# Kernel optimization log

Hardware: AMD Instinct MI355X
Metric: run time of the kernel (lower is better)

## Reference

```python
import math
import jax, jax.numpy as jnp
import numpy as np

D_MODEL = 1024
N_HEADS = 16
D_K = D_MODEL // N_HEADS


def _alibi_slopes(n_heads):
    # Faithful to the torch _get_slopes: slopes[i] = 2**(-8 + i), subsampled if
    # n_heads is not a power of two.
    power = 2 ** math.ceil(math.log2(n_heads))
    slopes = np.array([2.0 ** (-8 + i) for i in range(power)], dtype=np.float32)
    if n_heads != power:
        ratio = power // n_heads
        slopes = slopes[np.arange(0, power, ratio)][:n_heads]
    return jnp.asarray(slopes)


def setup_inputs() -> dict:
    key = jax.random.key(0)
    ks = jax.random.split(key, 11)
    B, S, D = 2, 2048, D_MODEL
    w = 0.02  # weight init scale
    return {
        "query": jax.random.normal(ks[0], (B, S, D), jnp.float32),
        "key": jax.random.normal(ks[1], (B, S, D), jnp.float32),
        "value": jax.random.normal(ks[2], (B, S, D), jnp.float32),
        "Wq": jax.random.normal(ks[3], (D, D), jnp.float32) * w,
        "bq": jax.random.normal(ks[4], (D,), jnp.float32) * w,
        "Wk": jax.random.normal(ks[5], (D, D), jnp.float32) * w,
        "bk": jax.random.normal(ks[6], (D,), jnp.float32) * w,
        "Wv": jax.random.normal(ks[7], (D, D), jnp.float32) * w,
        "bv": jax.random.normal(ks[8], (D,), jnp.float32) * w,
        "Wo": jax.random.normal(ks[9], (D, D), jnp.float32) * w,
        "bo": jax.random.normal(ks[10], (D,), jnp.float32) * w,
    }


def reference(query, key, value, Wq, bq, Wk, bk, Wv, bv, Wo, bo):
    B, Sq, D = query.shape
    Sk = key.shape[1]
    H, dk = N_HEADS, D_K

    # projections (torch Linear: x @ W.T + b)
    q = (query @ Wq.T + bq).reshape(B, Sq, H, dk).transpose(0, 2, 1, 3)  # [B,H,Sq,dk]
    k = (key @ Wk.T + bk).reshape(B, Sk, H, dk).transpose(0, 2, 1, 3)    # [B,H,Sk,dk]
    v = (value @ Wv.T + bv).reshape(B, Sk, H, dk).transpose(0, 2, 1, 3)  # [B,H,Sk,dk]

    scores = jnp.einsum("bhqd,bhkd->bhqk", q, k) / jnp.sqrt(jnp.float32(dk))

    # ALiBi bias: slopes[h] * (i - j), non-causal path (is_causal=False)
    dist = (jnp.arange(Sq)[:, None] - jnp.arange(Sk)[None, :]).astype(scores.dtype)
    slopes = _alibi_slopes(H)
    scores = scores + slopes[None, :, None, None] * dist[None, None, :, :]

    attn = jax.nn.softmax(scores, axis=-1)
    out = jnp.einsum("bhqk,bhkd->bhqd", attn, v)          # [B,H,Sq,dk]
    out = out.transpose(0, 2, 1, 3).reshape(B, Sq, D)     # [B,Sq,D]
    return out @ Wo.T + bo
```

## Files before the change

kernel.cpp:

```cpp
#include <hip/hip_runtime.h>

typedef __bf16 bf16_t;
typedef bf16_t bf16x8 __attribute__((ext_vector_type(8)));
typedef float f32x4 __attribute__((ext_vector_type(4)));
typedef float f32x16 __attribute__((ext_vector_type(16)));
typedef unsigned short u16x4 __attribute__((ext_vector_type(4)));
typedef unsigned int u32x4v __attribute__((ext_vector_type(4)));
typedef unsigned int u32;

#define DEV static __device__ __forceinline__


DEV unsigned short f2bf(float f) {
  unsigned int u = __builtin_bit_cast(unsigned int, f);
  u = (u + 0x7fffu + ((u >> 16) & 1u)) >> 16;
  return (unsigned short)u;
}

DEV float fexp2(float x) {
  float r;
  asm("v_exp_f32 %0, %1" : "=v"(r) : "v"(x));
  return r;
}

DEV u32 cvtpk(float lo, float hi_) {
  u32 r;
  asm("v_cvt_pk_bf16_f32 %0, %1, %2" : "=v"(r) : "v"(lo), "v"(hi_));
  return r;
}

DEV void plswap(u32& a, u32& b) {
  asm("v_permlane32_swap_b32 %0, %1" : "+v"(a), "+v"(b));
}

DEV void async_ld16(const unsigned short* gsrc, unsigned short* lbase, int lane) {
#if __has_builtin(__builtin_amdgcn_global_load_lds)
  __builtin_amdgcn_global_load_lds(
      (const __attribute__((address_space(1))) unsigned int*)(const void*)gsrc,
      (__attribute__((address_space(3))) unsigned int*)(void*)lbase, 16, 0, 0);
#else
  *reinterpret_cast<u32x4v*>(reinterpret_cast<char*>(lbase) + lane * 16) =
      *reinterpret_cast<const u32x4v*>(gsrc);
#endif
}


DEV void cvt_body(const float* __restrict__ src, unsigned short* __restrict__ dst, int i) {
  const float4* s = reinterpret_cast<const float4*>(src) + (size_t)i * 2;
  float4 a = s[0], c = s[1];
  u16x4 lo = {f2bf(a.x), f2bf(a.y), f2bf(a.z), f2bf(a.w)};
  u16x4 hi = {f2bf(c.x), f2bf(c.y), f2bf(c.z), f2bf(c.w)};
  u16x4* d = reinterpret_cast<u16x4*>(dst) + (size_t)i * 2;
  d[0] = lo;
  d[1] = hi;
}

__global__ __launch_bounds__(256) void cvt_qkv(const float* __restrict__ q,
                                               const float* __restrict__ k,
                                               const float* __restrict__ v,
                                               unsigned short* dq, unsigned short* dk,
                                               unsigned short* dv) {
  const int i = blockIdx.x * 256 + threadIdx.x;
  const float* src = blockIdx.z == 0 ? q : blockIdx.z == 1 ? k : v;
  unsigned short* dst = blockIdx.z == 0 ? dq : blockIdx.z == 1 ? dk : dv;
  cvt_body(src, dst, i);
}

__global__ __launch_bounds__(256) void cvt_w(const float* __restrict__ a,
                                             const float* __restrict__ b,
                                             const float* __restrict__ c,
                                             const float* __restrict__ d, unsigned short* da,
                                             unsigned short* db_, unsigned short* dc,
                                             unsigned short* dd) {
  const int i = blockIdx.x * 256 + threadIdx.x;
  const float* src = blockIdx.z == 0 ? a : blockIdx.z == 1 ? b : blockIdx.z == 2 ? c : d;
  unsigned short* dst = blockIdx.z == 0 ? da : blockIdx.z == 1 ? db_ : blockIdx.z == 2 ? dc : dd;
  cvt_body(src, dst, i);
}


DEV void stage_tile_128x64(const unsigned short* __restrict__ G, int row0, int k0,
                           unsigned short* lbuf, int lane, int wv) {
#pragma unroll
  for (int r = 0; r < 4; ++r) {
    const int rowA = (r * 4 + wv) * 8 + (lane >> 3);
    const int chunk = (lane & 7) ^ (rowA & 7);
    const unsigned short* gsrc = G + (size_t)(row0 + rowA) * 1024 + k0 + chunk * 8;
    unsigned short* lbase = lbuf + (r * 4 + wv) * 512;
    async_ld16(gsrc, lbase, lane);
  }
}

DEV void gemm_core(const unsigned short* __restrict__ X, const unsigned short* __restrict__ W,
                   unsigned short* lA0, unsigned short* lA1, unsigned short* lB0,
                   unsigned short* lB1, int bm0, int bn0, int lane, int wv, int wm, int wn,
                   f32x4 acc[4][4]) {
  stage_tile_128x64(X, bm0, 0, lA0, lane, wv);
  stage_tile_128x64(W, bn0, 0, lB0, lane, wv);
  __syncthreads();
  for (int kt = 0; kt < 16; ++kt) {
    unsigned short* lA = (kt & 1) ? lA1 : lA0;
    unsigned short* lB = (kt & 1) ? lB1 : lB0;
    unsigned short* nA = (kt & 1) ? lA0 : lA1;
    unsigned short* nB = (kt & 1) ? lB0 : lB1;
    if (kt < 15) {
      stage_tile_128x64(X, bm0, (kt + 1) * 64, nA, lane, wv);
      stage_tile_128x64(W, bn0, (kt + 1) * 64, nB, lane, wv);
    }
#pragma unroll
    for (int kk = 0; kk < 2; ++kk) {
      bf16x8 af[4], bfr[4];
#pragma unroll
      for (int f = 0; f < 4; ++f) {
        const int rowA = wm * 64 + f * 16 + (lane & 15);
        const int cA = (kk * 4 + (lane >> 4)) ^ (rowA & 7);
        af[f] = *reinterpret_cast<const bf16x8*>(lA + rowA * 64 + cA * 8);
        const int rowB = wn * 64 + f * 16 + (lane & 15);
        const int cB = (kk * 4 + (lane >> 4)) ^ (rowB & 7);
        bfr[f] = *reinterpret_cast<const bf16x8*>(lB + rowB * 64 + cB * 8);
      }
#pragma unroll
      for (int i = 0; i < 4; ++i)
#pragma unroll
        for (int j = 0; j < 4; ++j)
          acc[i][j] = __builtin_amdgcn_mfma_f32_16x16x32_bf16(af[i], bfr[j], acc[i][j], 0, 0, 0);
    }
    __syncthreads();
  }
}


__global__ __launch_bounds__(256) void gemm_qkv_kernel(
    const unsigned short* __restrict__ Xq, const unsigned short* __restrict__ Xk,
    const unsigned short* __restrict__ Xv, const unsigned short* __restrict__ Wq,
    const unsigned short* __restrict__ Wk, const unsigned short* __restrict__ Wv,
    const float* __restrict__ bq, const float* __restrict__ bk, const float* __restrict__ bv,
    unsigned short* __restrict__ Qp, unsigned short* __restrict__ Kp,
    unsigned short* __restrict__ Vp) {
  __shared__ unsigned short lA[2][128 * 64];
  __shared__ unsigned short lB[2][128 * 64];
  const unsigned short* X;
  const unsigned short* W;
  const float* bias;
  unsigned short* dst;
  if (blockIdx.z == 0) { X = Xq; W = Wq; bias = bq; dst = Qp; }
  else if (blockIdx.z == 1) { X = Xk; W = Wk; bias = bk; dst = Kp; }
  else { X = Xv; W = Wv; bias = bv; dst = Vp; }
  const bool zV = (blockIdx.z == 2);
  const int lane = threadIdx.x & 63, wv = threadIdx.x >> 6;
  const int wm = wv >> 1, wn = wv & 1;
  const int bm0 = blockIdx.x * 128, bn0 = blockIdx.y * 128;
  f32x4 acc[4][4] = {};
  gemm_core(X, W, lA[0], lA[1], lB[0], lB[1], bm0, bn0, lane, wv, wm, wn, acc);
#pragma unroll
  for (int i = 0; i < 4; ++i) {
    const int mbase = bm0 + wm * 64 + i * 16 + ((lane >> 4) << 2);
#pragma unroll
    for (int j = 0; j < 4; ++j) {
      const int n = bn0 + wn * 64 + j * 16 + (lane & 15);
      const float bia = bias[n];
      const int h = n >> 6, d = n & 63;
#pragma unroll
      for (int r = 0; r < 4; ++r) {
        const int m = mbase + r;
        const int b = m >> 11, s = m & 2047;
        const unsigned short val = f2bf(acc[i][j][r] + bia);
        if (zV)
          dst[((size_t)(b * 16 + h) * 64 + d) * 2048 + s] = val;
        else
          dst[((size_t)(b * 16 + h) * 2048 + s) * 64 + d] = val;
      }
    }
  }
}


__global__ __launch_bounds__(256) void gemm_out_kernel(const unsigned short* __restrict__ X,
                                                       const unsigned short* __restrict__ W,
                                                       const float* __restrict__ bias,
                                                       float* __restrict__ out) {
  __shared__ unsigned short lA[2][128 * 64];
  __shared__ unsigned short lB[2][128 * 64];
  const int lane = threadIdx.x & 63, wv = threadIdx.x >> 6;
  const int wm = wv >> 1, wn = wv & 1;
  const int bm0 = blockIdx.x * 128, bn0 = blockIdx.y * 128;
  f32x4 acc[4][4] = {};
  gemm_core(X, W, lA[0], lA[1], lB[0], lB[1], bm0, bn0, lane, wv, wm, wn, acc);
#pragma unroll
  for (int i = 0; i < 4; ++i) {
    const int mbase = bm0 + wm * 64 + i * 16 + ((lane >> 4) << 2);
#pragma unroll
    for (int j = 0; j < 4; ++j) {
      const int n = bn0 + wn * 64 + j * 16 + (lane & 15);
      const float bia = bias[n];
#pragma unroll
      for (int r = 0; r < 4; ++r) out[(size_t)(mbase + r) * 1024 + n] = acc[i][j][r] + bia;
    }
  }
}


__global__ __launch_bounds__(256) void knorm_kernel(const unsigned short* __restrict__ Kp,
                                                    unsigned* __restrict__ nb2) {
  const int bh = blockIdx.y;
  const int s = blockIdx.x * 256 + threadIdx.x;
  const u32x4v* row = reinterpret_cast<const u32x4v*>(Kp + ((size_t)bh * 2048 + s) * 64);
  float ss = 0.0f;
#pragma unroll
  for (int c = 0; c < 8; ++c) {
    u32x4v u = row[c];
#pragma unroll
    for (int e = 0; e < 4; ++e) {
      const float lo = __builtin_bit_cast(float, u[e] << 16);
      const float hi = __builtin_bit_cast(float, u[e] & 0xFFFF0000u);
      ss = __builtin_fmaf(lo, lo, ss);
      ss = __builtin_fmaf(hi, hi, ss);
    }
  }
#pragma unroll
  for (int off = 1; off <= 32; off <<= 1) ss = fmaxf(ss, __shfl_xor(ss, off));
  if ((threadIdx.x & 63) == 0) atomicMax(nb2 + bh, __float_as_uint(ss));
}


__global__ __launch_bounds__(128) void attn_prepass(const unsigned short* __restrict__ Qp,
                                                    const unsigned short* __restrict__ Kp,
                                                    const unsigned* __restrict__ nb2,
                                                    float* __restrict__ mfA,
                                                    float* __restrict__ bltA) {
  __shared__ float sred[4];
  const int lane = threadIdx.x & 63, wv = threadIdx.x >> 6;
  const int lq = lane & 31, hi = lane >> 5;
  const int qt = blockIdx.x, bh = blockIdx.y, h = bh & 15;
  const float L2E = 1.4426950408889634f;
  const float slope2 = ldexpf(L2E, h - 8);
  const float SC2 = 0.125f * L2E;
  const size_t headoff = (size_t)bh * 2048 * 64;
  const unsigned short* Qh = Qp + headoff;
  const unsigned short* Kh = Kp + headoff;
  const int q_glob = qt * 64 + wv * 32 + lq;

  bf16x8 qf[4];
#pragma unroll
  for (int tt = 0; tt < 4; ++tt)
    qf[tt] = *reinterpret_cast<const bf16x8*>(Qh + (size_t)q_glob * 64 + tt * 16 + hi * 8);

  float qq = 0.0f;
#pragma unroll
  for (int tt = 0; tt < 4; ++tt)
#pragma unroll
    for (int e = 0; e < 8; ++e) {
      const float x = (float)qf[tt][e];
      qq = __builtin_fmaf(x, x, qq);
    }
  qq += __shfl_xor(qq, 32);
#pragma unroll
  for (int off = 1; off <= 16; off <<= 1) qq = fmaxf(qq, __shfl_xor(qq, off));

  f32x16 s0 = {}, s1 = {};
#pragma unroll
  for (int tt = 0; tt < 4; ++tt) {
    bf16x8 k0 = *reinterpret_cast<const bf16x8*>(Kh + (size_t)lq * 64 + tt * 16 + hi * 8);
    s0 = __builtin_amdgcn_mfma_f32_32x32x16_bf16(k0, qf[tt], s0, 0, 0, 0);
    bf16x8 k1 = *reinterpret_cast<const bf16x8*>(Kh + (size_t)(32 + lq) * 64 + tt * 16 + hi * 8);
    s1 = __builtin_amdgcn_mfma_f32_32x32x16_bf16(k1, qf[tt], s1, 0, 0, 0);
  }
  float zmax = -3.0e38f;
#pragma unroll
  for (int r = 0; r < 16; ++r) {
    const float cb = -slope2 * (float)(4 * hi + (r & 3) + 8 * (r >> 2));
    const float x0 = __builtin_fmaf(s0[r], SC2, cb);
    const float x1 = __builtin_fmaf(s1[r], SC2, cb - slope2 * 32.0f);
    zmax = fmaxf(zmax, fmaxf(x0, x1));
  }
  zmax = fmaxf(zmax, __shfl_xor(zmax, 32));
  float zmin = zmax;
#pragma unroll
  for (int off = 1; off <= 16; off <<= 1) zmin = fminf(zmin, __shfl_xor(zmin, off));
  if (lane == 0) {
    sred[wv] = zmin;
    sred[2 + wv] = qq;
  }
  __syncthreads();
  if (threadIdx.x == 0) {
    const float mf = fminf(sred[0], sred[1]);
    const float qn = sqrtf(fmaxf(sred[2], sred[3]));
    const float nk = sqrtf(__uint_as_float(nb2[bh]));
    mfA[bh * 32 + qt] = mf;
    bltA[bh * 32 + qt] = qn * nk * SC2;
  }
}


DEV void stage_tile64(const unsigned short* __restrict__ Gbase, size_t stride, int colbase,
                      unsigned short* lbuf, int lane, int wv) {
#pragma unroll
  for (int i = 0; i < 4; ++i) {
    const int r = i * 16 + wv * 8 + (lane >> 3);
    const int chunk = (lane & 7) ^ (r & 7);
    async_ld16(Gbase + (size_t)r * stride + colbase + chunk * 8, lbuf + (i * 16 + wv * 8) * 64,
               lane);
  }
}

__global__ __launch_bounds__(128) void attn_split_kernel(
    const unsigned short* __restrict__ Qp, const unsigned short* __restrict__ Kp,
    const unsigned short* __restrict__ VTp, const float* __restrict__ mfA,
    const float* __restrict__ bltA, float* __restrict__ ML, float* __restrict__ Opart, int Ct,
    int nsplit) {
  __shared__ unsigned short Kb[2][64 * 64];
  __shared__ unsigned short Vb[2][64 * 64];
  const int lane = threadIdx.x & 63, wv = threadIdx.x >> 6;
  const int lq = lane & 31, hi = lane >> 5;
  const int qt = blockIdx.x, sp = blockIdx.y, bh = blockIdx.z;
  const int h = bh & 15;
  const int idx = bh * 32 + qt;
  const float L2E = 1.4426950408889634f;
  const float slope2 = ldexpf(L2E, h - 8);
  const float SC2 = 0.125f * L2E;
  const float m_floor = mfA[idx], blt = bltA[idx];
  const float tf = (blt - m_floor + 34.0f) / (slope2 * 64.0f);
  const int T_act = min(32, (int)tf + 1);
  const int t0 = sp * Ct;
  const int nt = min(Ct, T_act - t0);
  float* mlb = ML + ((size_t)idx * nsplit + sp) * 128;
  if (nt <= 0) {
    mlb[threadIdx.x] = threadIdx.x < 64 ? -3.0e38f : 0.0f;
    return;
  }
  float* ob = Opart + ((size_t)idx * nsplit + sp) * 4096;
  const size_t headoff = (size_t)bh * 2048 * 64;
  const unsigned short* Qh = Qp + headoff;
  const unsigned short* Kh = Kp + headoff;
  const unsigned short* VTh = VTp + headoff;
  const int q_glob = qt * 64 + wv * 32 + lq;

  float cb0[16], cb1[16];
#pragma unroll
  for (int r = 0; r < 16; ++r) {
    cb0[r] = -slope2 * (float)(4 * hi + (r & 3) + 8 * (r >> 2));
    cb1[r] = cb0[r] - slope2 * 32.0f;
  }

  bf16x8 qf[4];
#pragma unroll
  for (int tt = 0; tt < 4; ++tt)
    qf[tt] = *reinterpret_cast<const bf16x8*>(Qh + (size_t)q_glob * 64 + tt * 16 + hi * 8);

  stage_tile64(Kh + (size_t)(t0 * 64) * 64, 64, 0, Kb[0], lane, wv);
  stage_tile64(VTh, 2048, t0 * 64, Vb[0], lane, wv);
  __syncthreads();

  f32x16 acc0 = {}, acc1 = {};
  float m_run = m_floor, l_run = 0.0f;

  for (int ti = 0; ti < nt; ++ti) {
    const int kv0 = (t0 + ti) * 64;
    const float s2k = slope2 * (float)kv0;
    const unsigned short* Kc = Kb[ti & 1];
    const unsigned short* Vc = Vb[ti & 1];
    if (ti + 1 < nt) {
      stage_tile64(Kh + (size_t)(kv0 + 64) * 64, 64, 0, Kb[(ti + 1) & 1], lane, wv);
      stage_tile64(VTh, 2048, kv0 + 64, Vb[(ti + 1) & 1], lane, wv);
    }
    f32x16 s0 = {}, s1 = {};
    __builtin_amdgcn_s_setprio(1);
#pragma unroll
    for (int tt = 0; tt < 4; ++tt) {
      {
        const int row = lq;
        const int ch = (tt * 2 + hi) ^ (row & 7);
        bf16x8 kf = *reinterpret_cast<const bf16x8*>(Kc + row * 64 + ch * 8);
        s0 = __builtin_amdgcn_mfma_f32_32x32x16_bf16(kf, qf[tt], s0, 0, 0, 0);
      }
      {
        const int row = 32 + lq;
        const int ch = (tt * 2 + hi) ^ (row & 7);
        bf16x8 kf = *reinterpret_cast<const bf16x8*>(Kc + row * 64 + ch * 8);
        s1 = __builtin_amdgcn_mfma_f32_32x32x16_bf16(kf, qf[tt], s1, 0, 0, 0);
      }
    }
    __builtin_amdgcn_s_setprio(0);
    float zmax = -3.0e38f;
#pragma unroll
    for (int r = 0; r < 16; ++r) {
      s0[r] = __builtin_fmaf(s0[r], SC2, cb0[r]);
      s1[r] = __builtin_fmaf(s1[r], SC2, cb1[r]);
      zmax = fmaxf(zmax, fmaxf(s0[r], s1[r]));
    }
    zmax = fmaxf(zmax, __shfl_xor(zmax, 32));
    const float tmax_true = zmax - s2k;
    if (__any(tmax_true > m_run + 8.0f)) {
      const float m_new = fmaxf(m_run, tmax_true);
      const float alpha = fexp2(m_run - m_new);
      m_run = m_new;
      l_run *= alpha;
      acc0 *= alpha;
      acc1 *= alpha;
    }
    const float mm = m_run + s2k;
    float ps0 = 0.0f, ps1 = 0.0f;
#pragma unroll
    for (int r = 0; r < 16; ++r) {
      const float p0 = fexp2(s0[r] - mm);
      const float p1 = fexp2(s1[r] - mm);
      s0[r] = p0;
      s1[r] = p1;
      ps0 += p0;
      ps1 += p1;
    }
    float psum = ps0 + ps1;
    psum += __shfl_xor(psum, 32);
    l_run += psum;
    bf16x8 pf[4];
#pragma unroll
    for (int half = 0; half < 2; ++half) {
      u32 w0 = cvtpk(s0[half * 8 + 0], s0[half * 8 + 1]);
      u32 w2 = cvtpk(s0[half * 8 + 4], s0[half * 8 + 5]);
      plswap(w0, w2);
      u32 w1 = cvtpk(s0[half * 8 + 2], s0[half * 8 + 3]);
      u32 w3 = cvtpk(s0[half * 8 + 6], s0[half * 8 + 7]);
      plswap(w1, w3);
      u32x4v ww = {w0, w1, w2, w3};
      pf[half] = __builtin_bit_cast(bf16x8, ww);
    }
#pragma unroll
    for (int half = 0; half < 2; ++half) {
      u32 w0 = cvtpk(s1[half * 8 + 0], s1[half * 8 + 1]);
      u32 w2 = cvtpk(s1[half * 8 + 4], s1[half * 8 + 5]);
      plswap(w0, w2);
      u32 w1 = cvtpk(s1[half * 8 + 2], s1[half * 8 + 3]);
      u32 w3 = cvtpk(s1[half * 8 + 6], s1[half * 8 + 7]);
      plswap(w1, w3);
      u32x4v ww = {w0, w1, w2, w3};
      pf[2 + half] = __builtin_bit_cast(bf16x8, ww);
    }
    __builtin_amdgcn_s_setprio(1);
#pragma unroll
    for (int tt = 0; tt < 4; ++tt) {
      {
        const int row = lq;
        const int ch = (tt * 2 + hi) ^ (row & 7);
        bf16x8 vf = *reinterpret_cast<const bf16x8*>(Vc + row * 64 + ch * 8);
        acc0 = __builtin_amdgcn_mfma_f32_32x32x16_bf16(vf, pf[tt], acc0, 0, 0, 0);
      }
      {
        const int row = 32 + lq;
        const int ch = (tt * 2 + hi) ^ (row & 7);
        bf16x8 vf = *reinterpret_cast<const bf16x8*>(Vc + row * 64 + ch * 8);
        acc1 = __builtin_amdgcn_mfma_f32_32x32x16_bf16(vf, pf[tt], acc1, 0, 0, 0);
      }
    }
    __builtin_amdgcn_s_setprio(0);
    __syncthreads();
  }
  const int qloc = wv * 32 + lq;
  if (hi == 0) {
    mlb[qloc] = m_run;
    mlb[64 + qloc] = l_run;
  }
#pragma unroll
  for (int g = 0; g < 4; ++g) {
    f32x4 w0, w1;
#pragma unroll
    for (int e = 0; e < 4; ++e) {
      w0[e] = acc0[g * 4 + e];
      w1[e] = acc1[g * 4 + e];
    }
    *reinterpret_cast<f32x4*>(ob + qloc * 64 + g * 8 + 4 * hi) = w0;
    *reinterpret_cast<f32x4*>(ob + qloc * 64 + 32 + g * 8 + 4 * hi) = w1;
  }
}


__global__ __launch_bounds__(256) void attn_combine(const float* __restrict__ ML,
                                                    const float* __restrict__ Opart,
                                                    unsigned short* __restrict__ Ob, int nsplit) {
  const int idx = blockIdx.x;
  const int bh = idx >> 5, qt = idx & 31;
  const int h = bh & 15, b = bh >> 4;
  const int q = threadIdx.x >> 2, d0 = (threadIdx.x & 3) * 16;
  const float* mlb = ML + (size_t)idx * nsplit * 128;
  const float* ob = Opart + (size_t)idx * nsplit * 4096;
  float m_g = -3.0e38f;
  for (int s = 0; s < nsplit; ++s) m_g = fmaxf(m_g, mlb[s * 128 + q]);
  float l = 0.0f;
  f32x4 acc[4] = {};
  for (int s = 0; s < nsplit; ++s) {
    const float ms = mlb[s * 128 + q], ls = mlb[s * 128 + 64 + q];
    const float w = fexp2(ms - m_g);
    const float wl = w * ls;
    if (wl > 0.0f) {
      l += wl;
      const f32x4* src = reinterpret_cast<const f32x4*>(ob + (size_t)s * 4096 + q * 64 + d0);
#pragma unroll
      for (int j = 0; j < 4; ++j) {
        f32x4 v = src[j];
#pragma unroll
        for (int e = 0; e < 4; ++e) acc[j][e] = __builtin_fmaf(w, v[e], acc[j][e]);
      }
    }
  }
  const float invl = 1.0f / l;
  unsigned short* orow = Ob + ((size_t)(b * 2048 + qt * 64 + q)) * 1024 + h * 64 + d0;
#pragma unroll
  for (int j = 0; j < 4; ++j) {
    u16x4 pk;
#pragma unroll
    for (int e = 0; e < 4; ++e) pk[e] = f2bf(acc[j][e] * invl);
    *reinterpret_cast<u16x4*>(orow + j * 4) = pk;
  }
}


extern "C" void kernel_launch(void* const* d_in, const int* in_sizes, int n_in, void* d_out,
                              int out_size, void* d_ws, size_t ws_size, hipStream_t stream) {
  const float* q = (const float*)d_in[0];
  const float* k = (const float*)d_in[1];
  const float* v = (const float*)d_in[2];
  const float* Wq = (const float*)d_in[3];
  const float* bq = (const float*)d_in[4];
  const float* Wk = (const float*)d_in[5];
  const float* bk = (const float*)d_in[6];
  const float* Wv = (const float*)d_in[7];
  const float* bv = (const float*)d_in[8];
  const float* Wo = (const float*)d_in[9];
  const float* bo = (const float*)d_in[10];

  char* ws = (char*)d_ws;
  const size_t MB = 1024 * 1024;
  unsigned short* qb = (unsigned short*)(ws + 0 * MB);
  unsigned short* kb = (unsigned short*)(ws + 8 * MB);
  unsigned short* vb = (unsigned short*)(ws + 16 * MB);
  unsigned short* Wqb = (unsigned short*)(ws + 24 * MB);
  unsigned short* Wkb = (unsigned short*)(ws + 26 * MB);
  unsigned short* Wvb = (unsigned short*)(ws + 28 * MB);
  unsigned short* Wob = (unsigned short*)(ws + 30 * MB);
  unsigned short* Qp = (unsigned short*)(ws + 32 * MB);
  unsigned short* Kp = (unsigned short*)(ws + 40 * MB);
  unsigned short* VTp = (unsigned short*)(ws + 48 * MB);
  unsigned short* Obf = (unsigned short*)(ws + 0 * MB);

  int nsplit;
  float *nb2f, *mfA, *bltA, *ML, *Opart;
  if (ws_size >= (size_t)121 * MB) nsplit = 4;
  else if (ws_size >= (size_t)89 * MB) nsplit = 2;
  else nsplit = 1;
  if (ws_size >= (size_t)73 * MB) {
    nb2f = (float*)(ws + 24 * MB);
    mfA = (float*)(ws + 24 * MB + 4096);
    bltA = (float*)(ws + 24 * MB + 8192);
    ML = (float*)(ws + 26 * MB);
    Opart = (float*)(ws + 56 * MB);
  } else {
    nsplit = 1;
    nb2f = (float*)(ws + 26 * MB);
    mfA = (float*)(ws + 26 * MB + 4096);
    bltA = (float*)(ws + 26 * MB + 8192);
    ML = (float*)(ws + 26 * MB + 65536);
    Opart = (float*)(ws + 8 * MB);
  }
  const int Ct = 32 / nsplit;

  cvt_qkv<<<dim3(2048, 1, 3), 256, 0, stream>>>(q, k, v, qb, kb, vb);
  cvt_w<<<dim3(512, 1, 4), 256, 0, stream>>>(Wq, Wk, Wv, Wo, Wqb, Wkb, Wvb, Wob);

  gemm_qkv_kernel<<<dim3(32, 8, 3), 256, 0, stream>>>(qb, kb, vb, Wqb, Wkb, Wvb, bq, bk, bv, Qp,
                                                      Kp, VTp);
  hipMemsetAsync(nb2f, 0, 32 * sizeof(float), stream);
  knorm_kernel<<<dim3(8, 32), 256, 0, stream>>>(Kp, (unsigned*)nb2f);
  attn_prepass<<<dim3(32, 32), 128, 0, stream>>>(Qp, Kp, (const unsigned*)nb2f, mfA, bltA);
  attn_split_kernel<<<dim3(32, nsplit, 32), 128, 0, stream>>>(Qp, Kp, VTp, mfA, bltA, ML, Opart,
                                                              Ct, nsplit);
  attn_combine<<<1024, 256, 0, stream>>>(ML, Opart, Obf, nsplit);
  gemm_out_kernel<<<dim3(32, 8), 256, 0, stream>>>(Obf, Wob, bo, (float*)d_out);
}
```

Before: 131.0 us.

## Merge conversion kernels, shrink GEMM N-tile, swizzle blocks, fold K-norm into QKV GEMM

```diff
diff --git a/kernel.cpp b/kernel.cpp
--- a/kernel.cpp
+++ b/kernel.cpp
@@ -55,48 +55,58 @@
   d[1] = hi;
 }
 
-__global__ __launch_bounds__(256) void cvt_qkv(const float* __restrict__ q,
-                                               const float* __restrict__ k,
-                                               const float* __restrict__ v,
-                                               unsigned short* dq, unsigned short* dk,
-                                               unsigned short* dv) {
-  const int i = blockIdx.x * 256 + threadIdx.x;
-  const float* src = blockIdx.z == 0 ? q : blockIdx.z == 1 ? k : v;
-  unsigned short* dst = blockIdx.z == 0 ? dq : blockIdx.z == 1 ? dk : dv;
+__global__ __launch_bounds__(256) void cvt_all(
+    const float* __restrict__ q, const float* __restrict__ k, const float* __restrict__ v,
+    const float* __restrict__ Wq, const float* __restrict__ Wk, const float* __restrict__ Wv,
+    const float* __restrict__ Wo, unsigned short* dq, unsigned short* dk, unsigned short* dv,
+    unsigned short* dWq, unsigned short* dWk, unsigned short* dWv, unsigned short* dWo) {
+  const int bid = blockIdx.x;
+  const float* src;
+  unsigned short* dst;
+  int i;
+  if (bid < 6144) {
+    const int z = bid >> 11;
+    src = z == 0 ? q : z == 1 ? k : v;
+    dst = z == 0 ? dq : z == 1 ? dk : dv;
+    i = (bid & 2047) * 256 + threadIdx.x;
+  } else {
+    const int z = (bid - 6144) >> 9;
+    src = z == 0 ? Wq : z == 1 ? Wk : z == 2 ? Wv : Wo;
+    dst = z == 0 ? dWq : z == 1 ? dWk : z == 2 ? dWv : dWo;
+    i = ((bid - 6144) & 511) * 256 + threadIdx.x;
+  }
   cvt_body(src, dst, i);
 }
 
-__global__ __launch_bounds__(256) void cvt_w(const float* __restrict__ a,
-                                             const float* __restrict__ b,
-                                             const float* __restrict__ c,
-                                             const float* __restrict__ d, unsigned short* da,
-                                             unsigned short* db_, unsigned short* dc,
-                                             unsigned short* dd) {
-  const int i = blockIdx.x * 256 + threadIdx.x;
-  const float* src = blockIdx.z == 0 ? a : blockIdx.z == 1 ? b : blockIdx.z == 2 ? c : d;
-  unsigned short* dst = blockIdx.z == 0 ? da : blockIdx.z == 1 ? db_ : blockIdx.z == 2 ? dc : dd;
-  cvt_body(src, dst, i);
-}
-
-
-DEV void stage_tile_128x64(const unsigned short* __restrict__ G, int row0, int k0,
-                           unsigned short* lbuf, int lane, int wv) {
+
+DEV void stage_a128(const unsigned short* __restrict__ G, int row0, int k0,
+                    unsigned short* lbuf, int lane, int wv) {
 #pragma unroll
   for (int r = 0; r < 4; ++r) {
     const int rowA = (r * 4 + wv) * 8 + (lane >> 3);
     const int chunk = (lane & 7) ^ (rowA & 7);
-    const unsigned short* gsrc = G + (size_t)(row0 + rowA) * 1024 + k0 + chunk * 8;
-    unsigned short* lbase = lbuf + (r * 4 + wv) * 512;
-    async_ld16(gsrc, lbase, lane);
+    async_ld16(G + (size_t)(row0 + rowA) * 1024 + k0 + chunk * 8, lbuf + (r * 4 + wv) * 512,
+               lane);
+  }
+}
+
+DEV void stage_b64(const unsigned short* __restrict__ G, int row0, int k0,
+                   unsigned short* lbuf, int lane, int wv) {
+#pragma unroll
+  for (int r = 0; r < 2; ++r) {
+    const int rowB = (r * 4 + wv) * 8 + (lane >> 3);
+    const int chunk = (lane & 7) ^ (rowB & 7);
+    async_ld16(G + (size_t)(row0 + rowB) * 1024 + k0 + chunk * 8, lbuf + (r * 4 + wv) * 512,
+               lane);
   }
 }
 
 DEV void gemm_core(const unsigned short* __restrict__ X, const unsigned short* __restrict__ W,
                    unsigned short* lA0, unsigned short* lA1, unsigned short* lB0,
                    unsigned short* lB1, int bm0, int bn0, int lane, int wv, int wm, int wn,
-                   f32x4 acc[4][4]) {
-  stage_tile_128x64(X, bm0, 0, lA0, lane, wv);
-  stage_tile_128x64(W, bn0, 0, lB0, lane, wv);
+                   f32x4 acc[4][2]) {
+  stage_a128(X, bm0, 0, lA0, lane, wv);
+  stage_b64(W, bn0, 0, lB0, lane, wv);
   __syncthreads();
   for (int kt = 0; kt < 16; ++kt) {
     unsigned short* lA = (kt & 1) ? lA1 : lA0;
@@ -104,25 +114,28 @@
     unsigned short* nA = (kt & 1) ? lA0 : lA1;
     unsigned short* nB = (kt & 1) ? lB0 : lB1;
     if (kt < 15) {
-      stage_tile_128x64(X, bm0, (kt + 1) * 64, nA, lane, wv);
-      stage_tile_128x64(W, bn0, (kt + 1) * 64, nB, lane, wv);
+      stage_a128(X, bm0, (kt + 1) * 64, nA, lane, wv);
+      stage_b64(W, bn0, (kt + 1) * 64, nB, lane, wv);
     }
 #pragma unroll
     for (int kk = 0; kk < 2; ++kk) {
-      bf16x8 af[4], bfr[4];
+      bf16x8 af[4], bfr[2];
 #pragma unroll
       for (int f = 0; f < 4; ++f) {
         const int rowA = wm * 64 + f * 16 + (lane & 15);
         const int cA = (kk * 4 + (lane >> 4)) ^ (rowA & 7);
         af[f] = *reinterpret_cast<const bf16x8*>(lA + rowA * 64 + cA * 8);
-        const int rowB = wn * 64 + f * 16 + (lane & 15);
+      }
+#pragma unroll
+      for (int f = 0; f < 2; ++f) {
+        const int rowB = wn * 32 + f * 16 + (lane & 15);
         const int cB = (kk * 4 + (lane >> 4)) ^ (rowB & 7);
         bfr[f] = *reinterpret_cast<const bf16x8*>(lB + rowB * 64 + cB * 8);
       }
 #pragma unroll
       for (int i = 0; i < 4; ++i)
 #pragma unroll
-        for (int j = 0; j < 4; ++j)
+        for (int j = 0; j < 2; ++j)
           acc[i][j] = __builtin_amdgcn_mfma_f32_16x16x32_bf16(af[i], bfr[j], acc[i][j], 0, 0, 0);
     }
     __syncthreads();
@@ -130,68 +143,93 @@
 }
 
 
-__global__ __launch_bounds__(256) void gemm_qkv_kernel(
+__global__ __launch_bounds__(256, 3) void gemm_qkv_kernel(
     const unsigned short* __restrict__ Xq, const unsigned short* __restrict__ Xk,
     const unsigned short* __restrict__ Xv, const unsigned short* __restrict__ Wq,
     const unsigned short* __restrict__ Wk, const unsigned short* __restrict__ Wv,
     const float* __restrict__ bq, const float* __restrict__ bk, const float* __restrict__ bv,
     unsigned short* __restrict__ Qp, unsigned short* __restrict__ Kp,
-    unsigned short* __restrict__ Vp) {
-  __shared__ unsigned short lA[2][128 * 64];
-  __shared__ unsigned short lB[2][128 * 64];
+    unsigned short* __restrict__ Vp, unsigned* __restrict__ nb2) {
+  __shared__ unsigned short lA[2][8192];
+  __shared__ unsigned short lB[2][4096];
+  const int flat = blockIdx.x + 32 * blockIdx.y + 512 * blockIdx.z;
+  const int swz = (flat & 7) * 192 + (flat >> 3);
+  const int bx = swz & 31;
+  const int by = (swz >> 5) & 15;
+  const int bz = swz >> 9;
   const unsigned short* X;
   const unsigned short* W;
   const float* bias;
   unsigned short* dst;
-  if (blockIdx.z == 0) { X = Xq; W = Wq; bias = bq; dst = Qp; }
-  else if (blockIdx.z == 1) { X = Xk; W = Wk; bias = bk; dst = Kp; }
+  if (bz == 0) { X = Xq; W = Wq; bias = bq; dst = Qp; }
+  else if (bz == 1) { X = Xk; W = Wk; bias = bk; dst = Kp; }
   else { X = Xv; W = Wv; bias = bv; dst = Vp; }
-  const bool zV = (blockIdx.z == 2);
+  const bool zV = (bz == 2);
+  const bool zK = (bz == 1) && (nb2 != nullptr);
   const int lane = threadIdx.x & 63, wv = threadIdx.x >> 6;
   const int wm = wv >> 1, wn = wv & 1;
-  const int bm0 = blockIdx.x * 128, bn0 = blockIdx.y * 128;
-  f32x4 acc[4][4] = {};
+  const int bm0 = bx * 128, bn0 = by * 64;
+  f32x4 acc[4][2] = {};
   gemm_core(X, W, lA[0], lA[1], lB[0], lB[1], bm0, bn0, lane, wv, wm, wn, acc);
+  float rowmax = 0.0f;
 #pragma unroll
   for (int i = 0; i < 4; ++i) {
     const int mbase = bm0 + wm * 64 + i * 16 + ((lane >> 4) << 2);
 #pragma unroll
-    for (int j = 0; j < 4; ++j) {
-      const int n = bn0 + wn * 64 + j * 16 + (lane & 15);
-      const float bia = bias[n];
-      const int h = n >> 6, d = n & 63;
-#pragma unroll
-      for (int r = 0; r < 4; ++r) {
-        const int m = mbase + r;
-        const int b = m >> 11, s = m & 2047;
-        const unsigned short val = f2bf(acc[i][j][r] + bia);
+    for (int r = 0; r < 4; ++r) {
+      const int m = mbase + r;
+      const int b = m >> 11, s = m & 2047;
+      float ssp = 0.0f;
+#pragma unroll
+      for (int j = 0; j < 2; ++j) {
+        const int n = bn0 + wn * 32 + j * 16 + (lane & 15);
+        const float val = acc[i][j][r] + bias[n];
+        const unsigned short v16 = f2bf(val);
+        const int h = n >> 6, d = n & 63;
         if (zV)
-          dst[((size_t)(b * 16 + h) * 64 + d) * 2048 + s] = val;
+          dst[((size_t)(b * 16 + h) * 64 + d) * 2048 + s] = v16;
         else
-          dst[((size_t)(b * 16 + h) * 2048 + s) * 64 + d] = val;
-      }
-    }
-  }
-}
-
-
-__global__ __launch_bounds__(256) void gemm_out_kernel(const unsigned short* __restrict__ X,
-                                                       const unsigned short* __restrict__ W,
-                                                       const float* __restrict__ bias,
-                                                       float* __restrict__ out) {
-  __shared__ unsigned short lA[2][128 * 64];
-  __shared__ unsigned short lB[2][128 * 64];
+          dst[((size_t)(b * 16 + h) * 2048 + s) * 64 + d] = v16;
+        ssp = __builtin_fmaf(val, val, ssp);
+      }
+      if (zK) {
+        ssp += __shfl_xor(ssp, 1);
+        ssp += __shfl_xor(ssp, 2);
+        ssp += __shfl_xor(ssp, 4);
+        ssp += __shfl_xor(ssp, 8);
+        rowmax = fmaxf(rowmax, ssp);
+      }
+    }
+  }
+  if (zK) {
+    rowmax = fmaxf(rowmax, __shfl_xor(rowmax, 16));
+    rowmax = fmaxf(rowmax, __shfl_xor(rowmax, 32));
+    if (lane == 0)
+      atomicMax(nb2 + (((bm0 >> 11) * 16 + by) * 2 + wn), __float_as_uint(rowmax));
+  }
+}
+
+
+__global__ __launch_bounds__(256, 3) void gemm_out_kernel(const unsigned short* __restrict__ X,
+                                                          const unsigned short* __restrict__ W,
+                                                          const float* __restrict__ bias,
+                                                          float* __restrict__ out) {
+  __shared__ unsigned short lA[2][8192];
+  __shared__ unsigned short lB[2][4096];
+  const int flat = blockIdx.x + 32 * blockIdx.y;
+  const int swz = (flat & 7) * 64 + (flat >> 3);
+  const int bx = swz & 31, by = swz >> 5;
   const int lane = threadIdx.x & 63, wv = threadIdx.x >> 6;
   const int wm = wv >> 1, wn = wv & 1;
-  const int bm0 = blockIdx.x * 128, bn0 = blockIdx.y * 128;
-  f32x4 acc[4][4] = {};
+  const int bm0 = bx * 128, bn0 = by * 64;
+  f32x4 acc[4][2] = {};
   gemm_core(X, W, lA[0], lA[1], lB[0], lB[1], bm0, bn0, lane, wv, wm, wn, acc);
 #pragma unroll
   for (int i = 0; i < 4; ++i) {
     const int mbase = bm0 + wm * 64 + i * 16 + ((lane >> 4) << 2);
 #pragma unroll
-    for (int j = 0; j < 4; ++j) {
-      const int n = bn0 + wn * 64 + j * 16 + (lane & 15);
+    for (int j = 0; j < 2; ++j) {
+      const int n = bn0 + wn * 32 + j * 16 + (lane & 15);
       const float bia = bias[n];
 #pragma unroll
       for (int r = 0; r < 4; ++r) out[(size_t)(mbase + r) * 1024 + n] = acc[i][j][r] + bia;
@@ -205,21 +243,30 @@
   const int bh = blockIdx.y;
   const int s = blockIdx.x * 256 + threadIdx.x;
   const u32x4v* row = reinterpret_cast<const u32x4v*>(Kp + ((size_t)bh * 2048 + s) * 64);
-  float ss = 0.0f;
+  float ss0 = 0.0f, ss1 = 0.0f;
 #pragma unroll
   for (int c = 0; c < 8; ++c) {
     u32x4v u = row[c];
+    float acc = 0.0f;
 #pragma unroll
     for (int e = 0; e < 4; ++e) {
       const float lo = __builtin_bit_cast(float, u[e] << 16);
       const float hi = __builtin_bit_cast(float, u[e] & 0xFFFF0000u);
-      ss = __builtin_fmaf(lo, lo, ss);
-      ss = __builtin_fmaf(hi, hi, ss);
-    }
-  }
-#pragma unroll
-  for (int off = 1; off <= 32; off <<= 1) ss = fmaxf(ss, __shfl_xor(ss, off));
-  if ((threadIdx.x & 63) == 0) atomicMax(nb2 + bh, __float_as_uint(ss));
+      acc = __builtin_fmaf(lo, lo, acc);
+      acc = __builtin_fmaf(hi, hi, acc);
+    }
+    if (c < 4) ss0 += acc;
+    else ss1 += acc;
+  }
+#pragma unroll
+  for (int off = 1; off <= 32; off <<= 1) {
+    ss0 = fmaxf(ss0, __shfl_xor(ss0, off));
+    ss1 = fmaxf(ss1, __shfl_xor(ss1, off));
+  }
+  if ((threadIdx.x & 63) == 0) {
+    atomicMax(nb2 + bh * 2, __float_as_uint(ss0));
+    atomicMax(nb2 + bh * 2 + 1, __float_as_uint(ss1));
+  }
 }
 
 
@@ -285,7 +332,8 @@
   if (threadIdx.x == 0) {
     const float mf = fminf(sred[0], sred[1]);
     const float qn = sqrtf(fmaxf(sred[2], sred[3]));
-    const float nk = sqrtf(__uint_as_float(nb2[bh]));
+    const float nk2 = __uint_as_float(nb2[bh * 2]) + __uint_as_float(nb2[bh * 2 + 1]);
+    const float nk = sqrtf(nk2);
     mfA[bh * 32 + qt] = mf;
     bltA[bh * 32 + qt] = qn * nk * SC2;
   }
@@ -542,19 +590,23 @@
   unsigned short* Obf = (unsigned short*)(ws + 0 * MB);
 
   int nsplit;
-  float *nb2f, *mfA, *bltA, *ML, *Opart;
+  float *mfA, *bltA, *ML, *Opart;
+  unsigned* nb2;
+  bool fold_knorm;
   if (ws_size >= (size_t)121 * MB) nsplit = 4;
   else if (ws_size >= (size_t)89 * MB) nsplit = 2;
   else nsplit = 1;
   if (ws_size >= (size_t)73 * MB) {
-    nb2f = (float*)(ws + 24 * MB);
+    fold_knorm = true;
+    nb2 = (unsigned*)(ws + 56 * MB);
     mfA = (float*)(ws + 24 * MB + 4096);
     bltA = (float*)(ws + 24 * MB + 8192);
     ML = (float*)(ws + 26 * MB);
-    Opart = (float*)(ws + 56 * MB);
+    Opart = (float*)(ws + 56 * MB + 4096);
   } else {
+    fold_knorm = false;
     nsplit = 1;
-    nb2f = (float*)(ws + 26 * MB);
+    nb2 = (unsigned*)(ws + 26 * MB);
     mfA = (float*)(ws + 26 * MB + 4096);
     bltA = (float*)(ws + 26 * MB + 8192);
     ML = (float*)(ws + 26 * MB + 65536);
@@ -562,16 +614,14 @@
   }
   const int Ct = 32 / nsplit;
 
-  cvt_qkv<<<dim3(2048, 1, 3), 256, 0, stream>>>(q, k, v, qb, kb, vb);
-  cvt_w<<<dim3(512, 1, 4), 256, 0, stream>>>(Wq, Wk, Wv, Wo, Wqb, Wkb, Wvb, Wob);
-
-  gemm_qkv_kernel<<<dim3(32, 8, 3), 256, 0, stream>>>(qb, kb, vb, Wqb, Wkb, Wvb, bq, bk, bv, Qp,
-                                                      Kp, VTp);
-  hipMemsetAsync(nb2f, 0, 32 * sizeof(float), stream);
-  knorm_kernel<<<dim3(8, 32), 256, 0, stream>>>(Kp, (unsigned*)nb2f);
-  attn_prepass<<<dim3(32, 32), 128, 0, stream>>>(Qp, Kp, (const unsigned*)nb2f, mfA, bltA);
+  cvt_all<<<8192, 256, 0, stream>>>(q, k, v, Wq, Wk, Wv, Wo, qb, kb, vb, Wqb, Wkb, Wvb, Wob);
+  hipMemsetAsync(nb2, 0, 64 * sizeof(unsigned), stream);
+  gemm_qkv_kernel<<<dim3(32, 16, 3), 256, 0, stream>>>(qb, kb, vb, Wqb, Wkb, Wvb, bq, bk, bv, Qp,
+                                                       Kp, VTp, fold_knorm ? nb2 : nullptr);
+  if (!fold_knorm) knorm_kernel<<<dim3(8, 32), 256, 0, stream>>>(Kp, nb2);
+  attn_prepass<<<dim3(32, 32), 128, 0, stream>>>(Qp, Kp, nb2, mfA, bltA);
   attn_split_kernel<<<dim3(32, nsplit, 32), 128, 0, stream>>>(Qp, Kp, VTp, mfA, bltA, ML, Opart,
                                                               Ct, nsplit);
   attn_combine<<<1024, 256, 0, stream>>>(ML, Opart, Obf, nsplit);
-  gemm_out_kernel<<<dim3(32, 8), 256, 0, stream>>>(Obf, Wob, bo, (float*)d_out);
-}
+  gemm_out_kernel<<<dim3(32, 16), 256, 0, stream>>>(Obf, Wob, bo, (float*)d_out);
+}
```

Result: no change. 131.9 us (+0.7%).

## Fuse fp32-to-bf16 input conversion and K-norm reduction into QKV projection GEMM

Applied to the files above, without the earlier changes.

```diff
diff --git a/kernel.cpp b/kernel.cpp
--- a/kernel.cpp
+++ b/kernel.cpp
@@ -45,27 +45,6 @@
 }
 
 
-DEV void cvt_body(const float* __restrict__ src, unsigned short* __restrict__ dst, int i) {
-  const float4* s = reinterpret_cast<const float4*>(src) + (size_t)i * 2;
-  float4 a = s[0], c = s[1];
-  u16x4 lo = {f2bf(a.x), f2bf(a.y), f2bf(a.z), f2bf(a.w)};
-  u16x4 hi = {f2bf(c.x), f2bf(c.y), f2bf(c.z), f2bf(c.w)};
-  u16x4* d = reinterpret_cast<u16x4*>(dst) + (size_t)i * 2;
-  d[0] = lo;
-  d[1] = hi;
-}
-
-__global__ __launch_bounds__(256) void cvt_qkv(const float* __restrict__ q,
-                                               const float* __restrict__ k,
-                                               const float* __restrict__ v,
-                                               unsigned short* dq, unsigned short* dk,
-                                               unsigned short* dv) {
-  const int i = blockIdx.x * 256 + threadIdx.x;
-  const float* src = blockIdx.z == 0 ? q : blockIdx.z == 1 ? k : v;
-  unsigned short* dst = blockIdx.z == 0 ? dq : blockIdx.z == 1 ? dk : dv;
-  cvt_body(src, dst, i);
-}
-
 __global__ __launch_bounds__(256) void cvt_w(const float* __restrict__ a,
                                              const float* __restrict__ b,
                                              const float* __restrict__ c,
@@ -75,28 +54,83 @@
   const int i = blockIdx.x * 256 + threadIdx.x;
   const float* src = blockIdx.z == 0 ? a : blockIdx.z == 1 ? b : blockIdx.z == 2 ? c : d;
   unsigned short* dst = blockIdx.z == 0 ? da : blockIdx.z == 1 ? db_ : blockIdx.z == 2 ? dc : dd;
-  cvt_body(src, dst, i);
-}
-
-
-DEV void stage_tile_128x64(const unsigned short* __restrict__ G, int row0, int k0,
-                           unsigned short* lbuf, int lane, int wv) {
+  const float4* s = reinterpret_cast<const float4*>(src) + (size_t)i * 2;
+  float4 x = s[0], y = s[1];
+  u16x4 lo = {f2bf(x.x), f2bf(x.y), f2bf(x.z), f2bf(x.w)};
+  u16x4 hi = {f2bf(y.x), f2bf(y.y), f2bf(y.z), f2bf(y.w)};
+  u16x4* dptr = reinterpret_cast<u16x4*>(dst) + (size_t)i * 2;
+  dptr[0] = lo;
+  dptr[1] = hi;
+}
+
+
+DEV void stage_b128(const unsigned short* __restrict__ G, int row0, int k0,
+                    unsigned short* lbuf, int lane, int wv) {
 #pragma unroll
   for (int r = 0; r < 4; ++r) {
-    const int rowA = (r * 4 + wv) * 8 + (lane >> 3);
-    const int chunk = (lane & 7) ^ (rowA & 7);
-    const unsigned short* gsrc = G + (size_t)(row0 + rowA) * 1024 + k0 + chunk * 8;
-    unsigned short* lbase = lbuf + (r * 4 + wv) * 512;
-    async_ld16(gsrc, lbase, lane);
-  }
-}
-
-DEV void gemm_core(const unsigned short* __restrict__ X, const unsigned short* __restrict__ W,
-                   unsigned short* lA0, unsigned short* lA1, unsigned short* lB0,
-                   unsigned short* lB1, int bm0, int bn0, int lane, int wv, int wm, int wn,
+    const int rowB = (r * 4 + wv) * 8 + (lane >> 3);
+    const int chunk = (lane & 7) ^ (rowB & 7);
+    async_ld16(G + (size_t)(row0 + rowB) * 1024 + k0 + chunk * 8, lbuf + (r * 4 + wv) * 512,
+               lane);
+  }
+}
+
+DEV void stage_a_ld(const float* __restrict__ X, int row0, int k0, int lane, int wv,
+                    float4 rg[8]) {
+  const int r0 = lane >> 3, chunk = lane & 7;
+#pragma unroll
+  for (int c2 = 0; c2 < 4; ++c2) {
+    const float* g = X + (size_t)(row0 + wv * 32 + r0 + 8 * c2) * 1024 + k0 + chunk * 8;
+    rg[c2 * 2] = *reinterpret_cast<const float4*>(g);
+    rg[c2 * 2 + 1] = *reinterpret_cast<const float4*>(g + 4);
+  }
+}
+
+DEV void stage_a_wr(unsigned short* lbuf, int lane, int wv, const float4 rg[8]) {
+  const int r0 = lane >> 3, chunk = lane & 7;
+#pragma unroll
+  for (int c2 = 0; c2 < 4; ++c2) {
+    const int row = wv * 32 + r0 + 8 * c2;
+    const int p = chunk ^ (row & 7);
+    u32x4v w;
+    w[0] = cvtpk(rg[c2 * 2].x, rg[c2 * 2].y);
+    w[1] = cvtpk(rg[c2 * 2].z, rg[c2 * 2].w);
+    w[2] = cvtpk(rg[c2 * 2 + 1].x, rg[c2 * 2 + 1].y);
+    w[3] = cvtpk(rg[c2 * 2 + 1].z, rg[c2 * 2 + 1].w);
+    *reinterpret_cast<u32x4v*>(lbuf + row * 64 + p * 8) = w;
+  }
+}
+
+DEV void mfma_step(const unsigned short* lA, const unsigned short* lB, int lane, int wm, int wn,
                    f32x4 acc[4][4]) {
-  stage_tile_128x64(X, bm0, 0, lA0, lane, wv);
-  stage_tile_128x64(W, bn0, 0, lB0, lane, wv);
+#pragma unroll
+  for (int kk = 0; kk < 2; ++kk) {
+    bf16x8 af[4], bfr[4];
+#pragma unroll
+    for (int f = 0; f < 4; ++f) {
+      const int rowA = wm * 64 + f * 16 + (lane & 15);
+      const int cA = (kk * 4 + (lane >> 4)) ^ (rowA & 7);
+      af[f] = *reinterpret_cast<const bf16x8*>(lA + rowA * 64 + cA * 8);
+      const int rowB = wn * 64 + f * 16 + (lane & 15);
+      const int cB = (kk * 4 + (lane >> 4)) ^ (rowB & 7);
+      bfr[f] = *reinterpret_cast<const bf16x8*>(lB + rowB * 64 + cB * 8);
+    }
+#pragma unroll
+    for (int i = 0; i < 4; ++i)
+#pragma unroll
+      for (int j = 0; j < 4; ++j)
+        acc[i][j] = __builtin_amdgcn_mfma_f32_16x16x32_bf16(af[i], bfr[j], acc[i][j], 0, 0, 0);
+  }
+}
+
+DEV void gemm_core_f32a(const float* __restrict__ X, const unsigned short* __restrict__ W,
+                        unsigned short* lA0, unsigned short* lA1, unsigned short* lB0,
+                        unsigned short* lB1, int bm0, int bn0, int lane, int wv, int wm, int wn,
+                        f32x4 acc[4][4]) {
+  float4 rg[8];
+  stage_a_ld(X, bm0, 0, lane, wv, rg);
+  stage_b128(W, bn0, 0, lB0, lane, wv);
+  stage_a_wr(lA0, lane, wv, rg);
   __syncthreads();
   for (int kt = 0; kt < 16; ++kt) {
     unsigned short* lA = (kt & 1) ? lA1 : lA0;
@@ -104,72 +138,101 @@
     unsigned short* nA = (kt & 1) ? lA0 : lA1;
     unsigned short* nB = (kt & 1) ? lB0 : lB1;
     if (kt < 15) {
-      stage_tile_128x64(X, bm0, (kt + 1) * 64, nA, lane, wv);
-      stage_tile_128x64(W, bn0, (kt + 1) * 64, nB, lane, wv);
-    }
-#pragma unroll
-    for (int kk = 0; kk < 2; ++kk) {
-      bf16x8 af[4], bfr[4];
-#pragma unroll
-      for (int f = 0; f < 4; ++f) {
-        const int rowA = wm * 64 + f * 16 + (lane & 15);
-        const int cA = (kk * 4 + (lane >> 4)) ^ (rowA & 7);
-        af[f] = *reinterpret_cast<const bf16x8*>(lA + rowA * 64 + cA * 8);
-        const int rowB = wn * 64 + f * 16 + (lane & 15);
-        const int cB = (kk * 4 + (lane >> 4)) ^ (rowB & 7);
-        bfr[f] = *reinterpret_cast<const bf16x8*>(lB + rowB * 64 + cB * 8);
-      }
-#pragma unroll
-      for (int i = 0; i < 4; ++i)
-#pragma unroll
-        for (int j = 0; j < 4; ++j)
-          acc[i][j] = __builtin_amdgcn_mfma_f32_16x16x32_bf16(af[i], bfr[j], acc[i][j], 0, 0, 0);
-    }
+      stage_a_ld(X, bm0, (kt + 1) * 64, lane, wv, rg);
+      stage_b128(W, bn0, (kt + 1) * 64, nB, lane, wv);
+    }
+    mfma_step(lA, lB, lane, wm, wn, acc);
+    if (kt < 15) stage_a_wr(nA, lane, wv, rg);
     __syncthreads();
   }
 }
 
+DEV void gemm_core_bf16a(const unsigned short* __restrict__ X,
+                         const unsigned short* __restrict__ W, unsigned short* lA0,
+                         unsigned short* lA1, unsigned short* lB0, unsigned short* lB1, int bm0,
+                         int bn0, int lane, int wv, int wm, int wn, f32x4 acc[4][4]) {
+  stage_b128(X, bm0, 0, lA0, lane, wv);
+  stage_b128(W, bn0, 0, lB0, lane, wv);
+  __syncthreads();
+  for (int kt = 0; kt < 16; ++kt) {
+    unsigned short* lA = (kt & 1) ? lA1 : lA0;
+    unsigned short* lB = (kt & 1) ? lB1 : lB0;
+    unsigned short* nA = (kt & 1) ? lA0 : lA1;
+    unsigned short* nB = (kt & 1) ? lB0 : lB1;
+    if (kt < 15) {
+      stage_b128(X, bm0, (kt + 1) * 64, nA, lane, wv);
+      stage_b128(W, bn0, (kt + 1) * 64, nB, lane, wv);
+    }
+    mfma_step(lA, lB, lane, wm, wn, acc);
+    __syncthreads();
+  }
+}
+
 
 __global__ __launch_bounds__(256) void gemm_qkv_kernel(
-    const unsigned short* __restrict__ Xq, const unsigned short* __restrict__ Xk,
-    const unsigned short* __restrict__ Xv, const unsigned short* __restrict__ Wq,
-    const unsigned short* __restrict__ Wk, const unsigned short* __restrict__ Wv,
-    const float* __restrict__ bq, const float* __restrict__ bk, const float* __restrict__ bv,
-    unsigned short* __restrict__ Qp, unsigned short* __restrict__ Kp,
-    unsigned short* __restrict__ Vp) {
-  __shared__ unsigned short lA[2][128 * 64];
-  __shared__ unsigned short lB[2][128 * 64];
-  const unsigned short* X;
+    const float* __restrict__ Xq, const float* __restrict__ Xk, const float* __restrict__ Xv,
+    const unsigned short* __restrict__ Wq, const unsigned short* __restrict__ Wk,
+    const unsigned short* __restrict__ Wv, const float* __restrict__ bq,
+    const float* __restrict__ bk, const float* __restrict__ bv, unsigned short* __restrict__ Qp,
+    unsigned short* __restrict__ Kp, unsigned short* __restrict__ Vp,
+    unsigned* __restrict__ nb2) {
+  __shared__ unsigned short lA[2][8192];
+  __shared__ unsigned short lB[2][8192];
+  const int flat = blockIdx.x + 32 * blockIdx.y + 256 * blockIdx.z;
+  const int swz = (flat & 7) * 96 + (flat >> 3);
+  const int bx = swz & 31;
+  const int by = (swz >> 5) & 7;
+  const int bz = swz >> 8;
+  const float* X;
   const unsigned short* W;
   const float* bias;
   unsigned short* dst;
-  if (blockIdx.z == 0) { X = Xq; W = Wq; bias = bq; dst = Qp; }
-  else if (blockIdx.z == 1) { X = Xk; W = Wk; bias = bk; dst = Kp; }
+  if (bz == 0) { X = Xq; W = Wq; bias = bq; dst = Qp; }
+  else if (bz == 1) { X = Xk; W = Wk; bias = bk; dst = Kp; }
   else { X = Xv; W = Wv; bias = bv; dst = Vp; }
-  const bool zV = (blockIdx.z == 2);
+  const bool zV = (bz == 2);
+  const bool zK = (bz == 1) && (nb2 != nullptr);
   const int lane = threadIdx.x & 63, wv = threadIdx.x >> 6;
   const int wm = wv >> 1, wn = wv & 1;
-  const int bm0 = blockIdx.x * 128, bn0 = blockIdx.y * 128;
+  const int bm0 = bx * 128, bn0 = by * 128;
   f32x4 acc[4][4] = {};
-  gemm_core(X, W, lA[0], lA[1], lB[0], lB[1], bm0, bn0, lane, wv, wm, wn, acc);
+  gemm_core_f32a(X, W, lA[0], lA[1], lB[0], lB[1], bm0, bn0, lane, wv, wm, wn, acc);
+  float rowmax = 0.0f;
 #pragma unroll
   for (int i = 0; i < 4; ++i) {
     const int mbase = bm0 + wm * 64 + i * 16 + ((lane >> 4) << 2);
 #pragma unroll
-    for (int j = 0; j < 4; ++j) {
-      const int n = bn0 + wn * 64 + j * 16 + (lane & 15);
-      const float bia = bias[n];
-      const int h = n >> 6, d = n & 63;
-#pragma unroll
-      for (int r = 0; r < 4; ++r) {
-        const int m = mbase + r;
-        const int b = m >> 11, s = m & 2047;
-        const unsigned short val = f2bf(acc[i][j][r] + bia);
+    for (int r = 0; r < 4; ++r) {
+      const int m = mbase + r;
+      const int b = m >> 11, s = m & 2047;
+      float ssp = 0.0f;
+#pragma unroll
+      for (int j = 0; j < 4; ++j) {
+        const int n = bn0 + wn * 64 + j * 16 + (lane & 15);
+        const float val = acc[i][j][r] + bias[n];
+        const unsigned short v16 = f2bf(val);
+        const int h = n >> 6, d = n & 63;
         if (zV)
-          dst[((size_t)(b * 16 + h) * 64 + d) * 2048 + s] = val;
+          dst[((size_t)(b * 16 + h) * 64 + d) * 2048 + s] = v16;
         else
-          dst[((size_t)(b * 16 + h) * 2048 + s) * 64 + d] = val;
+          dst[((size_t)(b * 16 + h) * 2048 + s) * 64 + d] = v16;
+        ssp = __builtin_fmaf(val, val, ssp);
       }
+      if (zK) {
+        ssp += __shfl_xor(ssp, 1);
+        ssp += __shfl_xor(ssp, 2);
+        ssp += __shfl_xor(ssp, 4);
+        ssp += __shfl_xor(ssp, 8);
+        rowmax = fmaxf(rowmax, ssp);
+      }
+    }
+  }
+  if (zK) {
+    rowmax = fmaxf(rowmax, __shfl_xor(rowmax, 16));
+    rowmax = fmaxf(rowmax, __shfl_xor(rowmax, 32));
+    if (lane == 0) {
+      const int head = (bm0 >> 11) * 16 + by * 2 + wn;
+      atomicMax(nb2 + head, __float_as_uint(rowmax));
     }
   }
 }
@@ -179,13 +242,16 @@
                                                        const unsigned short* __restrict__ W,
                                                        const float* __restrict__ bias,
                                                        float* __restrict__ out) {
-  __shared__ unsigned short lA[2][128 * 64];
-  __shared__ unsigned short lB[2][128 * 64];
+  __shared__ unsigned short lA[2][8192];
+  __shared__ unsigned short lB[2][8192];
+  const int flat = blockIdx.x + 32 * blockIdx.y;
+  const int swz = (flat & 7) * 32 + (flat >> 3);
+  const int bx = swz & 31, by = swz >> 5;
   const int lane = threadIdx.x & 63, wv = threadIdx.x >> 6;
   const int wm = wv >> 1, wn = wv & 1;
-  const int bm0 = blockIdx.x * 128, bn0 = blockIdx.y * 128;
+  const int bm0 = bx * 128, bn0 = by * 128;
   f32x4 acc[4][4] = {};
-  gemm_core(X, W, lA[0], lA[1], lB[0], lB[1], bm0, bn0, lane, wv, wm, wn, acc);
+  gemm_core_bf16a(X, W, lA[0], lA[1], lB[0], lB[1], bm0, bn0, lane, wv, wm, wn, acc);
 #pragma unroll
   for (int i = 0; i < 4; ++i) {
     const int mbase = bm0 + wm * 64 + i * 16 + ((lane >> 4) << 2);
@@ -529,9 +595,6 @@
 
   char* ws = (char*)d_ws;
   const size_t MB = 1024 * 1024;
-  unsigned short* qb = (unsigned short*)(ws + 0 * MB);
-  unsigned short* kb = (unsigned short*)(ws + 8 * MB);
-  unsigned short* vb = (unsigned short*)(ws + 16 * MB);
   unsigned short* Wqb = (unsigned short*)(ws + 24 * MB);
   unsigned short* Wkb = (unsigned short*)(ws + 26 * MB);
   unsigned short* Wvb = (unsigned short*)(ws + 28 * MB);
@@ -542,19 +605,23 @@
   unsigned short* Obf = (unsigned short*)(ws + 0 * MB);
 
   int nsplit;
-  float *nb2f, *mfA, *bltA, *ML, *Opart;
+  float *mfA, *bltA, *ML, *Opart;
+  unsigned* nb2;
+  bool fold_knorm;
   if (ws_size >= (size_t)121 * MB) nsplit = 4;
   else if (ws_size >= (size_t)89 * MB) nsplit = 2;
   else nsplit = 1;
   if (ws_size >= (size_t)73 * MB) {
-    nb2f = (float*)(ws + 24 * MB);
+    fold_knorm = true;
+    nb2 = (unsigned*)(ws + 56 * MB);
     mfA = (float*)(ws + 24 * MB + 4096);
     bltA = (float*)(ws + 24 * MB + 8192);
-    ML = (float*)(ws + 26 * MB);
-    Opart = (float*)(ws + 56 * MB);
+    ML = (float*)(ws + 26 * MB + 65536);
+    Opart = (float*)(ws + 56 * MB + 4096);
   } else {
+    fold_knorm = false;
     nsplit = 1;
-    nb2f = (float*)(ws + 26 * MB);
+    nb2 = (unsigned*)(ws + 26 * MB);
     mfA = (float*)(ws + 26 * MB + 4096);
     bltA = (float*)(ws + 26 * MB + 8192);
     ML = (float*)(ws + 26 * MB + 65536);
@@ -562,14 +629,12 @@
   }
   const int Ct = 32 / nsplit;
 
-  cvt_qkv<<<dim3(2048, 1, 3), 256, 0, stream>>>(q, k, v, qb, kb, vb);
   cvt_w<<<dim3(512, 1, 4), 256, 0, stream>>>(Wq, Wk, Wv, Wo, Wqb, Wkb, Wvb, Wob);
-
-  gemm_qkv_kernel<<<dim3(32, 8, 3), 256, 0, stream>>>(qb, kb, vb, Wqb, Wkb, Wvb, bq, bk, bv, Qp,
-                                                      Kp, VTp);
-  hipMemsetAsync(nb2f, 0, 32 * sizeof(float), stream);
-  knorm_kernel<<<dim3(8, 32), 256, 0, stream>>>(Kp, (unsigned*)nb2f);
-  attn_prepass<<<dim3(32, 32), 128, 0, stream>>>(Qp, Kp, (const unsigned*)nb2f, mfA, bltA);
+  hipMemsetAsync(nb2, 0, 64 * sizeof(unsigned), stream);
+  gemm_qkv_kernel<<<dim3(32, 8, 3), 256, 0, stream>>>(q, k, v, Wqb, Wkb, Wvb, bq, bk, bv, Qp, Kp,
+                                                      VTp, fold_knorm ? nb2 : nullptr);
+  if (!fold_knorm) knorm_kernel<<<dim3(8, 32), 256, 0, stream>>>(Kp, nb2);
+  attn_prepass<<<dim3(32, 32), 128, 0, stream>>>(Qp, Kp, nb2, mfA, bltA);
   attn_split_kernel<<<dim3(32, nsplit, 32), 128, 0, stream>>>(Qp, Kp, VTp, mfA, bltA, ML, Opart,
                                                               Ct, nsplit);
   attn_combine<<<1024, 256, 0, stream>>>(ML, Opart, Obf, nsplit);
```

Measured after the change: 150.8 us. +15.1%, slower.
